# Kernel optimization log

Hardware: AMD Instinct MI355X
Metric: run time of the kernel (lower is better)

The kernel has to match this reference:

```python
import jax, jax.numpy as jnp
import numpy as np

EPS = 1e-6

def _layernorm(x, g, b):
    mu = jnp.mean(x, axis=-1, keepdims=True)
    var = jnp.mean(jnp.square(x - mu), axis=-1, keepdims=True)
    return (x - mu) * jax.lax.rsqrt(var + EPS) * g + b

def _mhsa(xq, xk, xv, mask, Wq, bq, Wk, bk, Wv, bv, Wo, bo, num_heads):
    B, Nq, D = xq.shape
    Nk = xk.shape[1]
    dh = D // num_heads
    # project then split heads: [B, N, D] -> [B, H, N, dh]
    def split(x, W, b, N):
        return (x @ W + b).reshape(B, N, num_heads, dh).transpose(0, 2, 1, 3)
    q = split(xq, Wq, bq, Nq)
    k = split(xk, Wk, bk, Nk)
    v = split(xv, Wv, bv, Nk)
    scores = jnp.einsum('bhnd,bhmd->bhnm', q, k) / jnp.sqrt(jnp.float32(dh))
    if mask is not None:
        scores = scores + mask * (-1e9)
    w = jax.nn.softmax(scores, axis=-1)
    out = jnp.einsum('bhnm,bhmd->bhnd', w, v)          # [B,H,Nq,dh]
    out = out.transpose(0, 2, 1, 3).reshape(B, Nq, D)  # concat heads
    return out @ Wo + bo

def setup_inputs() -> dict:
    B, N, D, FF = 2, 2048, 512, 2048
    key = jax.random.key(0)
    ks = jax.random.split(key, 32)
    std = 0.02
    p = {}
    p['inputs'] = jax.random.normal(ks[0], (B, N, D), jnp.float32)
    p['enc_output'] = jax.random.normal(ks[1], (B, N, D), jnp.float32)
    # causal look-ahead mask: 1 where masked (future positions)
    p['look_ahead_mask'] = jnp.triu(jnp.ones((N, N), jnp.float32), k=1)[None, None]
    p['padding_mask'] = jnp.zeros((B, 1, 1, N), jnp.float32)
    i = 2
    for pre in ('q1', 'k1', 'v1', 'o1', 'q2', 'k2', 'v2', 'o2'):
        p[pre + '_w'] = jax.random.normal(ks[i], (D, D), jnp.float32) * std; i += 1
        p[pre + '_b'] = jnp.zeros((D,), jnp.float32)
    p['f1_w'] = jax.random.normal(ks[i], (D, FF), jnp.float32) * std; i += 1
    p['f1_b'] = jnp.zeros((FF,), jnp.float32)
    p['f2_w'] = jax.random.normal(ks[i], (FF, D), jnp.float32) * std; i += 1
    p['f2_b'] = jnp.zeros((D,), jnp.float32)
    for ln in ('ln1', 'ln2', 'ln3'):
        p[ln + '_g'] = jnp.ones((D,), jnp.float32)
        p[ln + '_b'] = jnp.zeros((D,), jnp.float32)
    p['training'] = 0
    return p

def reference(inputs, enc_output, look_ahead_mask, padding_mask,
              q1_w, q1_b, k1_w, k1_b, v1_w, v1_b, o1_w, o1_b,
              q2_w, q2_b, k2_w, k2_b, v2_w, v2_b, o2_w, o2_b,
              f1_w, f1_b, f2_w, f2_b,
              ln1_g, ln1_b, ln2_g, ln2_b, ln3_g, ln3_b,
              training):
    H = 8
    # self-attention (q=k=v=inputs), causal mask; dropout inactive (eval)
    attn1 = _mhsa(inputs, inputs, inputs, look_ahead_mask,
                  q1_w, q1_b, k1_w, k1_b, v1_w, v1_b, o1_w, o1_b, H)
    out1 = _layernorm(inputs + attn1, ln1_g, ln1_b)
    # cross attention: NOTE original arg order -> q=enc, k=enc, v=out1
    attn2 = _mhsa(enc_output, enc_output, out1, padding_mask,
                  q2_w, q2_b, k2_w, k2_b, v2_w, v2_b, o2_w, o2_b, H)
    out2 = _layernorm(out1 + attn2, ln2_g, ln2_b)
    ffn = jax.nn.relu(out2 @ f1_w + f1_b) @ f2_w + f2_b
    return _layernorm(out2 + ffn, ln3_g, ln3_b)
```

## Files before the change

### kernel.cpp

```cpp
#include <hip/hip_runtime.h>

typedef __attribute__((ext_vector_type(8))) _Float16 half8;
typedef __attribute__((ext_vector_type(4))) _Float16 half4;
typedef __attribute__((ext_vector_type(2))) _Float16 half2_t;
typedef __attribute__((ext_vector_type(2))) __fp16 fp16x2;
typedef __attribute__((ext_vector_type(4))) float f32x4;

#define AS1 __attribute__((address_space(1)))
#define AS3 __attribute__((address_space(3)))

constexpr int SEQ = 2048, DM = 512, FFD = 2048, NH = 8, DH = 64;
constexpr int M = 2 * SEQ;
constexpr float QSCALE = 0.125f * 1.4426950408889634f;

__global__ __launch_bounds__(256)
void preproc(const float* __restrict__ q1_w, const float* __restrict__ k1_w,
             const float* __restrict__ v1_w, const float* __restrict__ o1_w,
             const float* __restrict__ q2_w, const float* __restrict__ k2_w,
             const float* __restrict__ v2_w, const float* __restrict__ o2_w,
             const float* __restrict__ f1_w, const float* __restrict__ f2_w,
             _Float16* __restrict__ qk1t, _Float16* __restrict__ v1t,
             _Float16* __restrict__ o1t, _Float16* __restrict__ qk2t,
             _Float16* __restrict__ v2t, _Float16* __restrict__ o2t,
             _Float16* __restrict__ f1t, _Float16* __restrict__ f2t,
             const float* __restrict__ q1_b, const float* __restrict__ k1_b,
             const float* __restrict__ q2_b, const float* __restrict__ k2_b,
             float* __restrict__ qk1b, float* __restrict__ qk2b,
             const float* __restrict__ inp, const float* __restrict__ enc,
             _Float16* __restrict__ xh, _Float16* __restrict__ eh) {
    __shared__ _Float16 tile[64 * 65];
    const int j = blockIdx.x, tid = threadIdx.x;
    if (j < 1024) {
        const float* src; _Float16* dst; int K, N, n0, k0;
        if (j < 512) {
            int w8 = j >> 6, t = j & 63;
            K = 512; N = 512; n0 = (t & 7) * 64; k0 = (t >> 3) * 64;
            switch (w8) {
                case 0: src = q1_w; dst = qk1t; break;
                case 1: src = k1_w; dst = qk1t + 512 * 512; break;
                case 2: src = v1_w; dst = v1t; break;
                case 3: src = o1_w; dst = o1t; break;
                case 4: src = q2_w; dst = qk2t; break;
                case 5: src = k2_w; dst = qk2t + 512 * 512; break;
                case 6: src = v2_w; dst = v2t; break;
                default: src = o2_w; dst = o2t; break;
            }
        } else if (j < 768) {
            int t = j - 512; K = 512; N = 2048;
            n0 = (t % 32) * 64; k0 = (t / 32) * 64; src = f1_w; dst = f1t;
        } else {
            int t = j - 768; K = 2048; N = 512;
            n0 = (t % 8) * 64; k0 = (t / 8) * 64; src = f2_w; dst = f2t;
        }
        int c = tid & 63, r4 = tid >> 6;
        for (int i = 0; i < 16; i++) {
            int r = r4 * 16 + i;
            tile[r * 65 + c] = (_Float16)src[(size_t)(k0 + r) * N + n0 + c];
        }
        __syncthreads();
        for (int i = 0; i < 16; i++) {
            int r = r4 * 16 + i;
            dst[(size_t)(n0 + r) * K + k0 + c] = tile[c * 65 + r];
        }
    } else if (j == 1024) {
        for (int i = tid; i < 512; i += 256) { qk1b[i] = q1_b[i]; qk1b[512 + i] = k1_b[i]; }
    } else if (j == 1025) {
        for (int i = tid; i < 512; i += 256) { qk2b[i] = q2_b[i]; qk2b[512 + i] = k2_b[i]; }
    } else {
        int k = j - 1026;
        const float* s = (k < 1024) ? inp : enc;
        _Float16* d = (k < 1024) ? xh : eh;
        size_t base = (size_t)(k & 1023) * 2048 + tid * 8;
        f32x4 a = *(const f32x4*)(s + base);
        f32x4 b2 = *(const f32x4*)(s + base + 4);
        half8 h;
        h[0] = (_Float16)a[0]; h[1] = (_Float16)a[1];
        h[2] = (_Float16)a[2]; h[3] = (_Float16)a[3];
        h[4] = (_Float16)b2[0]; h[5] = (_Float16)b2[1];
        h[6] = (_Float16)b2[2]; h[7] = (_Float16)b2[3];
        *(half8*)(d + base) = h;
    }
}

__global__ __launch_bounds__(256)
void qkv_gemm(const _Float16* __restrict__ xh, const _Float16* __restrict__ eh,
              const _Float16* __restrict__ qk1t, const _Float16* __restrict__ qk2t,
              const float* __restrict__ qk1b, const float* __restrict__ qk2b,
              _Float16* __restrict__ Qh1, _Float16* __restrict__ Kh1,
              _Float16* __restrict__ Qh2, _Float16* __restrict__ Kh2,
              const _Float16* __restrict__ v1t, const float* __restrict__ v1b,
              _Float16* __restrict__ V1T) {
    __shared__ _Float16 smem[192 * 64];
    const int tid = threadIdx.x;
    const int wid = tid >> 6, lid = tid & 63;
    const int wr = (wid & 1) * 64;
    const int wc = (wid >> 1) * 32;
    const int mi = lid & 15, qd = lid >> 4;
    const int jb = blockIdx.x;
    const _Float16 *Ap, *Bp;
    const float* bias;
    int m0, n0, epi, job = 0;
    if (jb < 1024) {
        epi = 4; job = jb >> 9;
        int L = jb & 511;
        int by = L % 32, bx = L / 32;
        m0 = by * 128; n0 = bx * 64;
        Ap = (job ? eh : xh) + (size_t)m0 * 512;
        Bp = (job ? qk2t : qk1t) + (size_t)n0 * 512;
        bias = job ? qk2b : qk1b;
    } else {
        epi = 3;
        int t = jb - 1024;
        int by = t & 3, bx = t >> 2;
        m0 = by * 128; n0 = bx * 64;
        Ap = v1t + (size_t)m0 * 512;
        Bp = xh + (size_t)n0 * 512;
        bias = v1b;
    }
    const int lrow = lid >> 3;
    const int gblk = (lid & 7) ^ ((lid >> 3) & 7);
    auto stage = [&](int kt) {
        #pragma unroll
        for (int l = 0; l < 4; l++) {
            int c = l * 4 + wid;
            int row = c * 8 + lrow;
            __builtin_amdgcn_global_load_lds(
                (const AS1 unsigned int*)(Ap + (size_t)row * 512 + kt * 64 + gblk * 8),
                (AS3 unsigned int*)&smem[c * 512], 16, 0, 0);
        }
        #pragma unroll
        for (int l = 0; l < 2; l++) {
            int c = l * 4 + wid;
            int row = c * 8 + lrow;
            __builtin_amdgcn_global_load_lds(
                (const AS1 unsigned int*)(Bp + (size_t)row * 512 + kt * 64 + gblk * 8),
                (AS3 unsigned int*)&smem[128 * 64 + c * 512], 16, 0, 0);
        }
    };
    f32x4 acc[4][2] = {};
    stage(0);
    __builtin_amdgcn_s_waitcnt(0x0F70);
    __syncthreads();
    for (int t = 0; t < 8; t++) {
        #pragma unroll
        for (int h = 0; h < 2; h++) {
            const int sA = ((4 * h + qd) ^ (mi & 7)) * 8;
            half8 af[4], bfr[2];
            #pragma unroll
            for (int i = 0; i < 4; i++)
                af[i] = *(const half8*)&smem[(wr + i * 16 + mi) * 64 + sA];
            #pragma unroll
            for (int j = 0; j < 2; j++)
                bfr[j] = *(const half8*)&smem[(128 + wc + j * 16 + mi) * 64 + sA];
            #pragma unroll
            for (int i = 0; i < 4; i++)
                #pragma unroll
                for (int j = 0; j < 2; j++)
                    acc[i][j] = __builtin_amdgcn_mfma_f32_16x16x32_f16(af[i], bfr[j], acc[i][j], 0, 0, 0);
        }
        if (t + 1 < 8) {
            __syncthreads();
            stage(t + 1);
            __builtin_amdgcn_s_waitcnt(0x0F70);
            __syncthreads();
        }
    }
    #pragma unroll
    for (int i = 0; i < 4; i++) {
        #pragma unroll
        for (int j = 0; j < 2; j++) {
            #pragma unroll
            for (int r = 0; r < 4; r++) {
                int row = m0 + wr + i * 16 + qd * 4 + r;
                int col = n0 + wc + j * 16 + mi;
                float v = acc[i][j][r];
                if (epi == 4) {
                    v += bias[col];
                    int hh2 = (col >> 6) & 7, d = col & 63;
                    int bb = row >> 11, nn = row & 2047;
                    size_t idx = (((size_t)bb * 8 + hh2) * SEQ + nn) * 64 + d;
                    if (col < 512) (job ? Qh2 : Qh1)[idx] = (_Float16)(v * QSCALE);
                    else           (job ? Kh2 : Kh1)[idx] = (_Float16)v;
                } else {
                    v += bias[row];
                    V1T[(size_t)row * 4096 + col] = (_Float16)v;
                }
            }
        }
    }
}

template<int BM, int BN, int WM, int WN, bool RELU, int EPI, int SPLIT>
__global__ __launch_bounds__(256)
void gemm_tn(const _Float16* __restrict__ A, const _Float16* __restrict__ Bt,
             const float* __restrict__ bias,
             float* __restrict__ outF, _Float16* __restrict__ outH,
             int Mtot, int N, int K) {
    constexpr int ROWS = BM + BN;
    __shared__ _Float16 smem[ROWS * 64];
    constexpr int AF = WM / 16, BF = WN / 16;
    constexpr int WROW = BM / WM;
    const int tid = threadIdx.x;
    const int wid = tid >> 6, lid = tid & 63;
    const int wr = (wid % WROW) * WM;
    const int wc = (wid / WROW) * WN;
    const int mi = lid & 15, qd = lid >> 4;
    const int gx = gridDim.x, gy = gridDim.y;
    const int L = blockIdx.y * gx + blockIdx.x;
    const int by = L % gy, bx = L / gy;
    const int m0 = by * BM, n0 = bx * BN;
    const int Kc = K / SPLIT;
    const int kbase = (SPLIT > 1) ? blockIdx.z * Kc : 0;
    const _Float16* Ap = A + (size_t)m0 * K + kbase;
    const _Float16* Bp = Bt + (size_t)n0 * K + kbase;
    const int lrow = lid >> 3;
    const int gblk = (lid & 7) ^ ((lid >> 3) & 7);
    auto stage = [&](int kt) {
        #pragma unroll
        for (int l = 0; l < BM / 32; l++) {
            int c = l * 4 + wid;
            int row = c * 8 + lrow;
            __builtin_amdgcn_global_load_lds(
                (const AS1 unsigned int*)(Ap + (size_t)row * K + kt * 64 + gblk * 8),
                (AS3 unsigned int*)&smem[c * 512], 16, 0, 0);
        }
        #pragma unroll
        for (int l = 0; l < BN / 32; l++) {
            int c = l * 4 + wid;
            int row = c * 8 + lrow;
            __builtin_amdgcn_global_load_lds(
                (const AS1 unsigned int*)(Bp + (size_t)row * K + kt * 64 + gblk * 8),
                (AS3 unsigned int*)&smem[BM * 64 + c * 512], 16, 0, 0);
        }
    };
    f32x4 acc[AF][BF] = {};
    const int NIT = Kc / 64;
    stage(0);
    __builtin_amdgcn_s_waitcnt(0x0F70);
    __syncthreads();
    for (int t = 0; t < NIT; t++) {
        #pragma unroll
        for (int h = 0; h < 2; h++) {
            const int sA = ((4 * h + qd) ^ (mi & 7)) * 8;
            half8 af[AF], bfr[BF];
            #pragma unroll
            for (int i = 0; i < AF; i++)
                af[i] = *(const half8*)&smem[(wr + i * 16 + mi) * 64 + sA];
            #pragma unroll
            for (int j = 0; j < BF; j++)
                bfr[j] = *(const half8*)&smem[(BM + wc + j * 16 + mi) * 64 + sA];
            #pragma unroll
            for (int i = 0; i < AF; i++)
                #pragma unroll
                for (int j = 0; j < BF; j++)
                    acc[i][j] = __builtin_amdgcn_mfma_f32_16x16x32_f16(af[i], bfr[j], acc[i][j], 0, 0, 0);
        }
        if (t + 1 < NIT) {
            __syncthreads();
            stage(t + 1);
            __builtin_amdgcn_s_waitcnt(0x0F70);
            __syncthreads();
        }
    }
    float* oF = outF;
    if (SPLIT > 1 && outF) oF = outF + (size_t)blockIdx.z * Mtot * N;
    _Float16* oH = outH;
    if (EPI == 5) oH = outH + (size_t)blockIdx.z * Mtot * N;
    const bool doBias = bias && (SPLIT == 1 || blockIdx.z == 0);
    #pragma unroll
    for (int i = 0; i < AF; i++) {
        #pragma unroll
        for (int j = 0; j < BF; j++) {
            #pragma unroll
            for (int r = 0; r < 4; r++) {
                int row = m0 + wr + i * 16 + qd * 4 + r;
                int col = n0 + wc + j * 16 + mi;
                float v = acc[i][j][r];
                if (EPI == 3) {
                    v += bias[row];
                    outH[(size_t)row * N + col] = (_Float16)v;
                } else if (EPI == 5) {
                    if (doBias) v += bias[col];
                    oH[(size_t)row * N + col] = (_Float16)v;
                } else {
                    if (doBias) v += bias[col];
                    if (RELU) v = fmaxf(v, 0.f);
                    size_t off = (size_t)row * N + col;
                    if (oF) oF[off] = v;
                    if (outH) outH[off] = (_Float16)v;
                }
            }
        }
    }
}

template<typename RT>
__global__ __launch_bounds__(256)
void oproj_ln(const _Float16* __restrict__ A, const _Float16* __restrict__ Bt,
              const float* __restrict__ bias, const RT* __restrict__ res,
              const float* __restrict__ lng, const float* __restrict__ lnb,
              _Float16* __restrict__ outH) {
    __shared__ _Float16 smem[66 * 512];
    __shared__ float sred[4][16], qred[4][16];
    const int tid = threadIdx.x;
    const int wid = tid >> 6, lid = tid & 63;
    const int mi = lid & 15, qd = lid >> 4;
    const int m0 = blockIdx.x * 16;
    const int wc = wid * 128;
    const _Float16* Ap = A + (size_t)m0 * 512;
    const int lrow = lid >> 3;
    const int gblk = (lid & 7) ^ ((lid >> 3) & 7);
    auto stage = [&](int kt) {
        if (wid < 2) {
            int row = wid * 8 + lrow;
            __builtin_amdgcn_global_load_lds(
                (const AS1 unsigned int*)(Ap + (size_t)row * 512 + kt * 64 + gblk * 8),
                (AS3 unsigned int*)&smem[wid * 512], 16, 0, 0);
        }
        #pragma unroll
        for (int l = 0; l < 16; l++) {
            int c = l * 4 + wid;
            int row = c * 8 + lrow;
            __builtin_amdgcn_global_load_lds(
                (const AS1 unsigned int*)(Bt + (size_t)row * 512 + kt * 64 + gblk * 8),
                (AS3 unsigned int*)&smem[(2 + c) * 512], 16, 0, 0);
        }
    };
    f32x4 acc[8] = {};
    stage(0);
    __builtin_amdgcn_s_waitcnt(0x0F70);
    __syncthreads();
    for (int t = 0; t < 8; t++) {
        #pragma unroll
        for (int h = 0; h < 2; h++) {
            const int sA = ((4 * h + qd) ^ (mi & 7)) * 8;
            half8 af = *(const half8*)&smem[mi * 64 + sA];
            half8 bfr[8];
            #pragma unroll
            for (int j = 0; j < 8; j++)
                bfr[j] = *(const half8*)&smem[1024 + (wc + j * 16 + mi) * 64 + sA];
            #pragma unroll
            for (int j = 0; j < 8; j++)
                acc[j] = __builtin_amdgcn_mfma_f32_16x16x32_f16(af, bfr[j], acc[j], 0, 0, 0);
        }
        if (t + 1 < 8) {
            __syncthreads();
            stage(t + 1);
            __builtin_amdgcn_s_waitcnt(0x0F70);
            __syncthreads();
        }
    }
    float ps[4] = {0.f, 0.f, 0.f, 0.f}, pq[4] = {0.f, 0.f, 0.f, 0.f};
    #pragma unroll
    for (int j = 0; j < 8; j++) {
        int col = wc + j * 16 + mi;
        float bj = bias[col];
        #pragma unroll
        for (int r = 0; r < 4; r++) {
            int row = m0 + qd * 4 + r;
            float x = acc[j][r] + bj + (float)res[(size_t)row * 512 + col];
            acc[j][r] = x;
            ps[r] += x; pq[r] += x * x;
        }
    }
    #pragma unroll
    for (int r = 0; r < 4; r++) {
        float s = ps[r], q = pq[r];
        s += __shfl_xor(s, 1, 64); q += __shfl_xor(q, 1, 64);
        s += __shfl_xor(s, 2, 64); q += __shfl_xor(q, 2, 64);
        s += __shfl_xor(s, 4, 64); q += __shfl_xor(q, 4, 64);
        s += __shfl_xor(s, 8, 64); q += __shfl_xor(q, 8, 64);
        if (mi == 0) { sred[wid][qd * 4 + r] = s; qred[wid][qd * 4 + r] = q; }
    }
    __syncthreads();
    #pragma unroll
    for (int r = 0; r < 4; r++) {
        int lr = qd * 4 + r;
        float ts = sred[0][lr] + sred[1][lr] + sred[2][lr] + sred[3][lr];
        float tq = qred[0][lr] + qred[1][lr] + qred[2][lr] + qred[3][lr];
        float mu = ts * (1.f / 512.f);
        float var = tq * (1.f / 512.f) - mu * mu;
        float rs = rsqrtf(var + 1e-6f);
        int row = m0 + lr;
        #pragma unroll
        for (int j = 0; j < 8; j++) {
            int col = wc + j * 16 + mi;
            float o = (acc[j][r] - mu) * rs * lng[col] + lnb[col];
            outH[(size_t)row * 512 + col] = (_Float16)o;
        }
    }
}

template<bool CAUSAL>
__global__ __launch_bounds__(512)
void attn_mono(const _Float16* __restrict__ Qh, const _Float16* __restrict__ Kh,
               const _Float16* __restrict__ VT, int ldv,
               _Float16* __restrict__ O) {
    const int x = blockIdx.x, bh = blockIdx.y;
    int qt;
    if (CAUSAL) {
        int half = x >> 1;
        int pick = (x & 1) ^ ((bh >> 3) & 1);
        qt = pick ? half : 31 - half;
    } else {
        qt = x;
    }
    const int nt = CAUSAL ? (qt + 1) : 32;
    const int np = (nt + 1) >> 1;
    __shared__ _Float16 Qs[64 * 64];
    __shared__ _Float16 Ps[2][64 * 64];
    __shared__ _Float16 Ks[2][64 * 64];
    __shared__ _Float16 Vs[2][64 * 64];
    __shared__ float Lsh[64];
    const int tid = threadIdx.x, w = tid >> 6, lane = tid & 63;
    const int w4 = w & 3, st = w >> 2;
    const int mi = lane & 15, qd = lane >> 4;
    const int qbase = qt * 64;
    const int b = bh >> 3, h = bh & 7;
    const _Float16* Qp = Qh + ((size_t)bh * SEQ + qbase) * 64;
    const _Float16* Kp = Kh + (size_t)bh * SEQ * 64;
    const _Float16* Vp = VT + (size_t)(h * 64) * ldv + (size_t)b * SEQ;
    const int lrow = lane >> 3;
    const int gblk = (lane & 7) ^ ((lane >> 3) & 7);
    const int f0 = (qd ^ (mi & 7)) * 8;
    const int f1 = ((qd + 4) ^ (mi & 7)) * 8;

    {
        int r0 = tid >> 3, blk = tid & 7;
        int sw = (blk ^ (r0 & 7)) * 8;
        half8 q0 = *(const half8*)(Qp + r0 * 64 + blk * 8);
        *(half8*)&Qs[r0 * 64 + sw] = q0;
    }
    __syncthreads();
    half8 qb0 = *(half8*)&Qs[(w4 * 16 + mi) * 64 + f0];
    half8 qb1 = *(half8*)&Qs[(w4 * 16 + mi) * 64 + f1];
    f32x4 oacc[4] = {};
    float lacc = 0.f;
    _Float16* Pst = Ps[st];

    for (int i = 0; i < np; i++) {
        const int t = 2 * i + st;
        const bool act = t < nt;
        __syncthreads();
        if (act) {
            #pragma unroll
            for (int l = 0; l < 2; l++) {
                int cc = l * 4 + w4;
                int row = cc * 8 + lrow;
                __builtin_amdgcn_global_load_lds(
                    (const AS1 unsigned int*)(Kp + ((size_t)(t * 64 + row)) * 64 + gblk * 8),
                    (AS3 unsigned int*)&Ks[st][cc * 512], 16, 0, 0);
                __builtin_amdgcn_global_load_lds(
                    (const AS1 unsigned int*)(Vp + (size_t)row * ldv + t * 64 + gblk * 8),
                    (AS3 unsigned int*)&Vs[st][cc * 512], 16, 0, 0);
            }
        }
        __builtin_amdgcn_s_waitcnt(0x0F70);
        __syncthreads();
        if (!act) continue;
        const _Float16* ksb = Ks[st];
        const _Float16* vsb = Vs[st];
        f32x4 s[4];
        #pragma unroll
        for (int j = 0; j < 4; j++) {
            half8 ka0 = *(const half8*)&ksb[(j * 16 + mi) * 64 + f0];
            half8 ka1 = *(const half8*)&ksb[(j * 16 + mi) * 64 + f1];
            f32x4 a = {};
            a = __builtin_amdgcn_mfma_f32_16x16x32_f16(ka0, qb0, a, 0, 0, 0);
            a = __builtin_amdgcn_mfma_f32_16x16x32_f16(ka1, qb1, a, 0, 0, 0);
            s[j] = a;
        }
        if (CAUSAL && t == qt) {
            int qg = qbase + w4 * 16 + mi;
            #pragma unroll
            for (int j = 0; j < 4; j++)
                #pragma unroll
                for (int r = 0; r < 4; r++) {
                    int key = t * 64 + j * 16 + qd * 4 + r;
                    if (key > qg) s[j][r] = -1e30f;
                }
        }
        #pragma unroll
        for (int j = 0; j < 4; j++)
            #pragma unroll
            for (int r = 0; r < 4; r++) {
                float pv = __builtin_amdgcn_exp2f(s[j][r]);
                s[j][r] = pv;
                lacc += pv;
            }
        #pragma unroll
        for (int j = 0; j < 4; j++) {
            fp16x2 lo = __builtin_amdgcn_cvt_pkrtz(s[j][0], s[j][1]);
            fp16x2 hi = __builtin_amdgcn_cvt_pkrtz(s[j][2], s[j][3]);
            half2_t lo2 = __builtin_bit_cast(half2_t, lo);
            half2_t hi2 = __builtin_bit_cast(half2_t, hi);
            half4 pq;
            pq[0] = lo2[0]; pq[1] = lo2[1]; pq[2] = hi2[0]; pq[3] = hi2[1];
            int blkp = (2 * j + (qd >> 1)) ^ (mi & 7);
            *(half4*)&Pst[(w4 * 16 + mi) * 64 + blkp * 8 + (qd & 1) * 4] = pq;
        }
        half8 pa0 = *(half8*)&Pst[(w4 * 16 + mi) * 64 + f0];
        half8 pa1 = *(half8*)&Pst[(w4 * 16 + mi) * 64 + f1];
        #pragma unroll
        for (int j = 0; j < 4; j++) {
            half8 vb0 = *(const half8*)&vsb[(j * 16 + mi) * 64 + f0];
            half8 vb1 = *(const half8*)&vsb[(j * 16 + mi) * 64 + f1];
            oacc[j] = __builtin_amdgcn_mfma_f32_16x16x32_f16(pa0, vb0, oacc[j], 0, 0, 0);
            oacc[j] = __builtin_amdgcn_mfma_f32_16x16x32_f16(pa1, vb1, oacc[j], 0, 0, 0);
        }
    }
    __syncthreads();
    if (st == 1) {
        float* obuf = (float*)Ks;
        float* lbuf = (float*)Vs;
        int base = (w4 * 64 + lane) * 16;
        #pragma unroll
        for (int j = 0; j < 4; j++)
            #pragma unroll
            for (int r = 0; r < 4; r++)
                obuf[base + j * 4 + r] = oacc[j][r];
        lbuf[w4 * 64 + lane] = lacc;
    }
    __syncthreads();
    if (st == 0) {
        const float* obuf = (const float*)Ks;
        const float* lbuf = (const float*)Vs;
        int base = (w4 * 64 + lane) * 16;
        #pragma unroll
        for (int j = 0; j < 4; j++)
            #pragma unroll
            for (int r = 0; r < 4; r++)
                oacc[j][r] += obuf[base + j * 4 + r];
        lacc += lbuf[w4 * 64 + lane];
        lacc += __shfl_xor(lacc, 16, 64);
        lacc += __shfl_xor(lacc, 32, 64);
        if (qd == 0) Lsh[w4 * 16 + mi] = lacc;
    }
    __syncthreads();
    if (st == 0) {
        #pragma unroll
        for (int r = 0; r < 4; r++) {
            float rl = 1.f / Lsh[w4 * 16 + qd * 4 + r];
            int qrow = qbase + w4 * 16 + qd * 4 + r;
            size_t obase = ((size_t)(b * SEQ + qrow)) * 512 + h * 64;
            #pragma unroll
            for (int j = 0; j < 4; j++)
                O[obase + j * 16 + mi] = (_Float16)(oacc[j][r] * rl);
        }
    }
}

template<typename RT>
__global__ __launch_bounds__(256)
void add_ln(const RT* __restrict__ res, const _Float16* __restrict__ y,
            size_t pstride, int nparts,
            const float* __restrict__ g, const float* __restrict__ bb,
            float* __restrict__ outF, _Float16* __restrict__ outH) {
    int row = blockIdx.x;
    int tid = threadIdx.x;
    size_t base = (size_t)row * 512;
    float x0 = (float)res[base + tid];
    float x1 = (float)res[base + tid + 256];
    for (int s = 0; s < nparts; s++) {
        x0 += (float)y[s * pstride + base + tid];
        x1 += (float)y[s * pstride + base + tid + 256];
    }
    float s = x0 + x1, sq = x0 * x0 + x1 * x1;
    #pragma unroll
    for (int off = 32; off > 0; off >>= 1) {
        s += __shfl_xor(s, off, 64);
        sq += __shfl_xor(sq, off, 64);
    }
    __shared__ float ls[4], lq[4];
    int w = tid >> 6;
    if ((tid & 63) == 0) { ls[w] = s; lq[w] = sq; }
    __syncthreads();
    s = ls[0] + ls[1] + ls[2] + ls[3];
    sq = lq[0] + lq[1] + lq[2] + lq[3];
    float mu = s * (1.f / 512.f);
    float var = sq * (1.f / 512.f) - mu * mu;
    float rs = rsqrtf(var + 1e-6f);
    float o0 = (x0 - mu) * rs * g[tid] + bb[tid];
    float o1 = (x1 - mu) * rs * g[tid + 256] + bb[tid + 256];
    if (outF) { outF[base + tid] = o0; outF[base + tid + 256] = o1; }
    if (outH) { outH[base + tid] = (_Float16)o0; outH[base + tid + 256] = (_Float16)o1; }
}

extern "C" void kernel_launch(void* const* d_in, const int* in_sizes, int n_in,
                              void* d_out, int out_size, void* d_ws, size_t ws_size,
                              hipStream_t stream) {
    (void)in_sizes; (void)n_in; (void)out_size; (void)ws_size;
    const float* inp  = (const float*)d_in[0];
    const float* enc  = (const float*)d_in[1];
    const float* q1_w = (const float*)d_in[4];
    const float* q1_b = (const float*)d_in[5];
    const float* k1_w = (const float*)d_in[6];
    const float* k1_b = (const float*)d_in[7];
    const float* v1_w = (const float*)d_in[8];
    const float* v1_b = (const float*)d_in[9];
    const float* o1_w = (const float*)d_in[10];
    const float* o1_b = (const float*)d_in[11];
    const float* q2_w = (const float*)d_in[12];
    const float* q2_b = (const float*)d_in[13];
    const float* k2_w = (const float*)d_in[14];
    const float* k2_b = (const float*)d_in[15];
    const float* v2_w = (const float*)d_in[16];
    const float* v2_b = (const float*)d_in[17];
    const float* o2_w = (const float*)d_in[18];
    const float* o2_b = (const float*)d_in[19];
    const float* f1_w = (const float*)d_in[20];
    const float* f1_b = (const float*)d_in[21];
    const float* f2_w = (const float*)d_in[22];
    const float* f2_b = (const float*)d_in[23];
    const float* ln1_g = (const float*)d_in[24];
    const float* ln1_b = (const float*)d_in[25];
    const float* ln2_g = (const float*)d_in[26];
    const float* ln2_b = (const float*)d_in[27];
    const float* ln3_g = (const float*)d_in[28];
    const float* ln3_b = (const float*)d_in[29];

    char* p = (char*)d_ws;
    auto alloc = [&](size_t bytes) { char* r = p; p += (bytes + 255) & ~(size_t)255; return (void*)r; };
    _Float16* xh    = (_Float16*)alloc((size_t)M * DM * 2);
    _Float16* eh    = (_Float16*)alloc((size_t)M * DM * 2);
    _Float16* qk1t  = (_Float16*)alloc((size_t)1024 * DM * 2);
    _Float16* v1t   = (_Float16*)alloc((size_t)DM * DM * 2);
    _Float16* o1t   = (_Float16*)alloc((size_t)DM * DM * 2);
    _Float16* qk2t  = (_Float16*)alloc((size_t)1024 * DM * 2);
    _Float16* v2t   = (_Float16*)alloc((size_t)DM * DM * 2);
    _Float16* o2t   = (_Float16*)alloc((size_t)DM * DM * 2);
    _Float16* f1t   = (_Float16*)alloc((size_t)FFD * DM * 2);
    _Float16* f2t   = (_Float16*)alloc((size_t)DM * FFD * 2);
    float* qk1b     = (float*)alloc(1024 * 4);
    float* qk2b     = (float*)alloc(1024 * 4);
    _Float16* Qh1   = (_Float16*)alloc((size_t)M * DM * 2);
    _Float16* Kh1   = (_Float16*)alloc((size_t)M * DM * 2);
    _Float16* Qh2   = (_Float16*)alloc((size_t)M * DM * 2);
    _Float16* Kh2   = (_Float16*)alloc((size_t)M * DM * 2);
    _Float16* V1T   = (_Float16*)alloc((size_t)DM * M * 2);
    _Float16* V2T   = (_Float16*)alloc((size_t)DM * M * 2);
    _Float16* Ah    = (_Float16*)alloc((size_t)M * DM * 2);
    _Float16* Ph    = (_Float16*)alloc((size_t)2 * M * DM * 2);
    _Float16* out1h = (_Float16*)alloc((size_t)M * DM * 2);
    _Float16* out2h = (_Float16*)alloc((size_t)M * DM * 2);
    _Float16* hh    = (_Float16*)alloc((size_t)M * FFD * 2);
    const size_t PS = (size_t)M * DM;

    dim3 t256(256), t512(512);
    preproc<<<dim3(1026 + 2048), t256, 0, stream>>>(
        q1_w, k1_w, v1_w, o1_w, q2_w, k2_w, v2_w, o2_w, f1_w, f2_w,
        qk1t, v1t, o1t, qk2t, v2t, o2t, f1t, f2t,
        q1_b, k1_b, q2_b, k2_b, qk1b, qk2b, inp, enc, xh, eh);

    qkv_gemm<<<dim3(1280), t256, 0, stream>>>(
        xh, eh, qk1t, qk2t, qk1b, qk2b, Qh1, Kh1, Qh2, Kh2, v1t, v1_b, V1T);

    attn_mono<true><<<dim3(32, 16), t512, 0, stream>>>(Qh1, Kh1, V1T, M, Ah);
    oproj_ln<float><<<dim3(256), t256, 0, stream>>>(
        Ah, o1t, o1_b, inp, ln1_g, ln1_b, out1h);

    gemm_tn<64, 64, 32, 32, false, 3, 1><<<dim3(64, 8), t256, 0, stream>>>(
        v2t, out1h, v2_b, nullptr, V2T, 512, M, 512);
    attn_mono<false><<<dim3(32, 16), t512, 0, stream>>>(Qh2, Kh2, V2T, M, Ah);
    oproj_ln<_Float16><<<dim3(256), t256, 0, stream>>>(
        Ah, o2t, o2_b, out1h, ln2_g, ln2_b, out2h);

    gemm_tn<128, 64, 64, 32, true, 0, 1><<<dim3(32, 32), t256, 0, stream>>>(
        out2h, f1t, f1_b, nullptr, hh, M, 2048, 512);
    gemm_tn<64, 64, 32, 32, false, 5, 2><<<dim3(8, 64, 2), t256, 0, stream>>>(
        hh, f2t, f2_b, nullptr, Ph, M, 512, 2048);
    add_ln<_Float16><<<dim3(M), t256, 0, stream>>>(out2h, Ph, PS, 2, ln3_g, ln3_b, (float*)d_out, nullptr);
}
```

Baseline: 291.7 us.

## Fuse FFN second GEMM with residual add and final layernorm

Templates the fused GEMM+layernorm kernel on the K dimension and uses it for the FFN down-projection (K=2048). This replaces the split-K GEMM that wrote two fp16 partials plus the separate add_ln kernel. It removes one launch and the round trip of the partial buffers through memory. In exchange there are only 256 blocks, each running a 32-step K loop that is not double-buffered, so the GPU may be underused and serialized on load latency.

```diff
diff --git a/kernel.cpp b/kernel.cpp
--- a/kernel.cpp
+++ b/kernel.cpp
@@ -294,12 +294,12 @@
     }
 }
 
-template<typename RT>
+template<int KK, typename RT>
 __global__ __launch_bounds__(256)
 void oproj_ln(const _Float16* __restrict__ A, const _Float16* __restrict__ Bt,
               const float* __restrict__ bias, const RT* __restrict__ res,
               const float* __restrict__ lng, const float* __restrict__ lnb,
-              _Float16* __restrict__ outH) {
+              float* __restrict__ outF, _Float16* __restrict__ outH) {
     __shared__ _Float16 smem[66 * 512];
     __shared__ float sred[4][16], qred[4][16];
     const int tid = threadIdx.x;
@@ -307,14 +307,14 @@
     const int mi = lid & 15, qd = lid >> 4;
     const int m0 = blockIdx.x * 16;
     const int wc = wid * 128;
-    const _Float16* Ap = A + (size_t)m0 * 512;
+    const _Float16* Ap = A + (size_t)m0 * KK;
     const int lrow = lid >> 3;
     const int gblk = (lid & 7) ^ ((lid >> 3) & 7);
     auto stage = [&](int kt) {
         if (wid < 2) {
             int row = wid * 8 + lrow;
             __builtin_amdgcn_global_load_lds(
-                (const AS1 unsigned int*)(Ap + (size_t)row * 512 + kt * 64 + gblk * 8),
+                (const AS1 unsigned int*)(Ap + (size_t)row * KK + kt * 64 + gblk * 8),
                 (AS3 unsigned int*)&smem[wid * 512], 16, 0, 0);
         }
         #pragma unroll
@@ -322,15 +322,16 @@
             int c = l * 4 + wid;
             int row = c * 8 + lrow;
             __builtin_amdgcn_global_load_lds(
-                (const AS1 unsigned int*)(Bt + (size_t)row * 512 + kt * 64 + gblk * 8),
+                (const AS1 unsigned int*)(Bt + (size_t)row * KK + kt * 64 + gblk * 8),
                 (AS3 unsigned int*)&smem[(2 + c) * 512], 16, 0, 0);
         }
     };
     f32x4 acc[8] = {};
+    constexpr int NIT = KK / 64;
     stage(0);
     __builtin_amdgcn_s_waitcnt(0x0F70);
     __syncthreads();
-    for (int t = 0; t < 8; t++) {
+    for (int t = 0; t < NIT; t++) {
         #pragma unroll
         for (int h = 0; h < 2; h++) {
             const int sA = ((4 * h + qd) ^ (mi & 7)) * 8;
@@ -343,7 +344,7 @@
             for (int j = 0; j < 8; j++)
                 acc[j] = __builtin_amdgcn_mfma_f32_16x16x32_f16(af, bfr[j], acc[j], 0, 0, 0);
         }
-        if (t + 1 < 8) {
+        if (t + 1 < NIT) {
             __syncthreads();
             stage(t + 1);
             __builtin_amdgcn_s_waitcnt(0x0F70);
@@ -386,7 +387,8 @@
         for (int j = 0; j < 8; j++) {
             int col = wc + j * 16 + mi;
             float o = (acc[j][r] - mu) * rs * lng[col] + lnb[col];
-            outH[(size_t)row * 512 + col] = (_Float16)o;
+            if (outF) outF[(size_t)row * 512 + col] = o;
+            if (outH) outH[(size_t)row * 512 + col] = (_Float16)o;
         }
     }
 }
@@ -548,42 +550,6 @@
                 O[obase + j * 16 + mi] = (_Float16)(oacc[j][r] * rl);
         }
     }
-}
-
-template<typename RT>
-__global__ __launch_bounds__(256)
-void add_ln(const RT* __restrict__ res, const _Float16* __restrict__ y,
-            size_t pstride, int nparts,
-            const float* __restrict__ g, const float* __restrict__ bb,
-            float* __restrict__ outF, _Float16* __restrict__ outH) {
-    int row = blockIdx.x;
-    int tid = threadIdx.x;
-    size_t base = (size_t)row * 512;
-    float x0 = (float)res[base + tid];
-    float x1 = (float)res[base + tid + 256];
-    for (int s = 0; s < nparts; s++) {
-        x0 += (float)y[s * pstride + base + tid];
-        x1 += (float)y[s * pstride + base + tid + 256];
-    }
-    float s = x0 + x1, sq = x0 * x0 + x1 * x1;
-    #pragma unroll
-    for (int off = 32; off > 0; off >>= 1) {
-        s += __shfl_xor(s, off, 64);
-        sq += __shfl_xor(sq, off, 64);
-    }
-    __shared__ float ls[4], lq[4];
-    int w = tid >> 6;
-    if ((tid & 63) == 0) { ls[w] = s; lq[w] = sq; }
-    __syncthreads();
-    s = ls[0] + ls[1] + ls[2] + ls[3];
-    sq = lq[0] + lq[1] + lq[2] + lq[3];
-    float mu = s * (1.f / 512.f);
-    float var = sq * (1.f / 512.f) - mu * mu;
-    float rs = rsqrtf(var + 1e-6f);
-    float o0 = (x0 - mu) * rs * g[tid] + bb[tid];
-    float o1 = (x1 - mu) * rs * g[tid + 256] + bb[tid + 256];
-    if (outF) { outF[base + tid] = o0; outF[base + tid + 256] = o1; }
-    if (outH) { outH[base + tid] = (_Float16)o0; outH[base + tid + 256] = (_Float16)o1; }
 }
 
 extern "C" void kernel_launch(void* const* d_in, const int* in_sizes, int n_in,
@@ -640,11 +606,9 @@
     _Float16* V1T   = (_Float16*)alloc((size_t)DM * M * 2);
     _Float16* V2T   = (_Float16*)alloc((size_t)DM * M * 2);
     _Float16* Ah    = (_Float16*)alloc((size_t)M * DM * 2);
-    _Float16* Ph    = (_Float16*)alloc((size_t)2 * M * DM * 2);
     _Float16* out1h = (_Float16*)alloc((size_t)M * DM * 2);
     _Float16* out2h = (_Float16*)alloc((size_t)M * DM * 2);
     _Float16* hh    = (_Float16*)alloc((size_t)M * FFD * 2);
-    const size_t PS = (size_t)M * DM;
 
     dim3 t256(256), t512(512);
     preproc<<<dim3(1026 + 2048), t256, 0, stream>>>(
@@ -656,18 +620,17 @@
         xh, eh, qk1t, qk2t, qk1b, qk2b, Qh1, Kh1, Qh2, Kh2, v1t, v1_b, V1T);
 
     attn_mono<true><<<dim3(32, 16), t512, 0, stream>>>(Qh1, Kh1, V1T, M, Ah);
-    oproj_ln<float><<<dim3(256), t256, 0, stream>>>(
-        Ah, o1t, o1_b, inp, ln1_g, ln1_b, out1h);
+    oproj_ln<512, float><<<dim3(256), t256, 0, stream>>>(
+        Ah, o1t, o1_b, inp, ln1_g, ln1_b, nullptr, out1h);
 
     gemm_tn<64, 64, 32, 32, false, 3, 1><<<dim3(64, 8), t256, 0, stream>>>(
         v2t, out1h, v2_b, nullptr, V2T, 512, M, 512);
     attn_mono<false><<<dim3(32, 16), t512, 0, stream>>>(Qh2, Kh2, V2T, M, Ah);
-    oproj_ln<_Float16><<<dim3(256), t256, 0, stream>>>(
-        Ah, o2t, o2_b, out1h, ln2_g, ln2_b, out2h);
+    oproj_ln<512, _Float16><<<dim3(256), t256, 0, stream>>>(
+        Ah, o2t, o2_b, out1h, ln2_g, ln2_b, nullptr, out2h);
 
     gemm_tn<128, 64, 64, 32, true, 0, 1><<<dim3(32, 32), t256, 0, stream>>>(
         out2h, f1t, f1_b, nullptr, hh, M, 2048, 512);
-    gemm_tn<64, 64, 32, 32, false, 5, 2><<<dim3(8, 64, 2), t256, 0, stream>>>(
-        hh, f2t, f2_b, nullptr, Ph, M, 512, 2048);
-    add_ln<_Float16><<<dim3(M), t256, 0, stream>>>(out2h, Ph, PS, 2, ln3_g, ln3_b, (float*)d_out, nullptr);
+    oproj_ln<2048, _Float16><<<dim3(256), t256, 0, stream>>>(
+        hh, f2t, f2_b, out2h, ln3_g, ln3_b, (float*)d_out, nullptr);
 }
```

After: 321.6 us. 1.1x slower.
